# Kernel tuning notes

Measured on AMD Instinct MI355X. Metric: run time of the kernel, lower is better.

## Reference

```python
import jax, jax.numpy as jnp
import numpy as np
from jax import lax

B, H, W = 16, 512, 512
K, C, D = 64, 512, 256  # num_clusters, feature channels, descriptor_dim


def conv2d(x, w, b, stride, pad):
    y = lax.conv_general_dilated(x, w, (stride, stride), ((pad, pad), (pad, pad)),
                                 dimension_numbers=("NCHW", "OIHW", "NCHW"))
    return y + b[None, :, None, None]


def maxpool2(x):
    return lax.reduce_window(x, -jnp.inf, lax.max, (1, 1, 2, 2), (1, 1, 2, 2), "VALID")


def setup_inputs() -> dict:
    key = jax.random.key(0)
    ks = jax.random.split(key, 16)
    def rn(k, shape, fan_in):
        return jax.random.normal(k, shape, jnp.float32) * (1.0 / np.sqrt(fan_in))
    return {
        "x": jax.random.normal(ks[0], (B, 3, H, W), jnp.float32),
        "w1": rn(ks[1], (64, 3, 3, 3), 27), "b1": jnp.zeros((64,), jnp.float32),
        "w2": rn(ks[2], (128, 64, 3, 3), 576), "b2": jnp.zeros((128,), jnp.float32),
        "w3": rn(ks[3], (256, 128, 3, 3), 1152), "b3": jnp.zeros((256,), jnp.float32),
        "w4": rn(ks[4], (512, 256, 3, 3), 2304), "b4": jnp.zeros((512,), jnp.float32),
        "wv": rn(ks[5], (K, C), C), "bv": jnp.zeros((K,), jnp.float32),
        "centroids": jax.random.normal(ks[6], (K, C), jnp.float32),
        "fw1": rn(ks[7], (D, K * C), K * C), "fb1": jnp.zeros((D,), jnp.float32),
        "fw2": rn(ks[8], (D, D), D), "fb2": jnp.zeros((D,), jnp.float32),
    }


def reference(x, w1, b1, w2, b2, w3, b3, w4, b4, wv, bv, centroids, fw1, fb1, fw2, fb2):
    # conv backbone (SimpleGlobalDescriptor.backbone)
    h = jax.nn.relu(conv2d(x, w1, b1, 2, 1)); h = maxpool2(h)
    h = jax.nn.relu(conv2d(h, w2, b2, 2, 1)); h = maxpool2(h)
    h = jax.nn.relu(conv2d(h, w3, b3, 2, 1)); h = maxpool2(h)
    h = jax.nn.relu(conv2d(h, w4, b4, 2, 1))
    feats = jnp.mean(h, axis=(2, 3))  # AdaptiveAvgPool2d((1,1)) -> (B, C)
    # NetVLAD soft assignment: 1x1 conv + softmax over cluster dim
    logits = jnp.einsum("bc,kc->bk", feats, wv) + bv  # (B, K)
    a = jax.nn.softmax(logits, axis=1)  # spatial N == 1 after avgpool
    # fused VLAD: a[:,k] * (feats - centroids[k]) summed over N(=1)
    # == a (outer) feats - a[:,:,None] * centroids
    vlad = a[:, :, None] * (feats[:, None, :] - centroids[None, :, :])  # (B, K, C)
    v = vlad.reshape(B, K * C)
    # final descriptor MLP + L2 norm
    d = jax.nn.relu(v @ fw1.T + fb1) @ fw2.T + fb2
    d = d / jnp.linalg.norm(d, axis=1, keepdims=True)
    return d
```

## Files before the change

### kernel.cpp

```cpp
#include <hip/hip_runtime.h>
#include <hip/hip_bf16.h>

typedef unsigned short ushort_t;
typedef short bf16x8 __attribute__((ext_vector_type(8)));
typedef float f32x4 __attribute__((ext_vector_type(4)));

__device__ __forceinline__ ushort_t f2b(float f) {
    __hip_bfloat16 h = __float2bfloat16(f);
    return *reinterpret_cast<ushort_t*>(&h);
}
__device__ __forceinline__ float b2f(short v) {
    union { unsigned int u; float f; } cv;
    cv.u = ((unsigned int)(ushort_t)v) << 16;
    return cv.f;
}

__global__ __launch_bounds__(256) void k_packall(const float* __restrict__ w1,
                                                 const float* __restrict__ w2,
                                                 const float* __restrict__ w3,
                                                 const float* __restrict__ w4,
                                                 ushort_t* __restrict__ o1,
                                                 ushort_t* __restrict__ o2,
                                                 ushort_t* __restrict__ o3,
                                                 ushort_t* __restrict__ o4m) {
    const int bx = blockIdx.x;
    if (bx < 512) {
        const int co = bx;
        __shared__ float sw[2304];
        for (int i = threadIdx.x; i < 2304; i += 256) sw[i] = w4[(size_t)co * 2304 + i];
        __syncthreads();
        const int g = co >> 4, l15 = co & 15;
        for (int it = threadIdx.x; it < 288; it += 256) {
            const int kc = it >> 2, kg = it & 3;
            const int k0 = kc * 32 + kg * 8;
            const int tap = k0 >> 8, ci0 = k0 & 255;
            const int lane = kg * 16 + l15;
            ushort_t tmp[8];
#pragma unroll
            for (int j = 0; j < 8; ++j)
                tmp[j] = f2b(sw[(ci0 + j) * 9 + tap]);
            *(float4*)(o4m + ((size_t)(kc * 32 + g) * 64 + lane) * 8) = *(const float4*)tmp;
        }
    } else if (bx < 656) {
        const int slot = (bx - 512) * 256 + threadIdx.x;
        const int lane = slot & 63, g = (slot >> 6) & 15, kc = slot >> 10;
        const int k0 = kc * 32 + ((lane >> 4) << 3);
        const int tap = k0 >> 7, cib = k0 & 127;
        const int ky = tap >= 6 ? 2 : (tap >= 3 ? 1 : 0), kx = tap - ky * 3;
        const int co = g * 16 + (lane & 15);
#pragma unroll
        for (int j = 0; j < 8; ++j)
            o3[slot * 8 + j] = f2b(w3[((co * 128 + cib + j) * 3 + ky) * 3 + kx]);
    } else if (bx < 692) {
        const int slot = (bx - 656) * 256 + threadIdx.x;
        const int lane = slot & 63, g = (slot >> 6) & 7, kc = slot >> 9;
        const int k0 = kc * 32 + ((lane >> 4) << 3);
        const int tap = k0 >> 6, sb = k0 & 63;
        const int ky = tap >= 6 ? 2 : (tap >= 3 ? 1 : 0), kx = tap - ky * 3;
        const int co = g * 16 + (lane & 15);
#pragma unroll
        for (int j = 0; j < 8; ++j) {
            const int s = sb + j;
            const int ci = 16 * (s & 3) + (s >> 2);
            o2[slot * 8 + j] = f2b(w2[((co * 64 + ci) * 3 + ky) * 3 + kx]);
        }
    } else {
        const int slot = threadIdx.x;
        const int lane = slot & 63, nf = slot >> 6;
        const int co = nf * 16 + (lane & 15);
        const int kg = lane >> 4;
#pragma unroll
        for (int j = 0; j < 8; ++j) {
            const int k = kg * 8 + j;
            float v = 0.f;
            if (k < 24) {
                const int ky = k >> 3, q = k & 7;
                const int kx = q / 3, c = q - 3 * kx;
                v = w1[(co * 3 + c) * 9 + ky * 3 + kx];
            } else if (k < 27) {
                const int ky = k - 24;
                v = w1[(co * 3 + 2) * 9 + ky * 3 + 2];
            }
            o1[slot * 8 + j] = f2b(v);
        }
    }
}

__global__ __launch_bounds__(256) void k_conv1f(const float* __restrict__ x,
                                                const ushort_t* __restrict__ wpk1,
                                                const float* __restrict__ b1,
                                                ushort_t* __restrict__ y1) {
    const int rp = blockIdx.x, xh = blockIdx.y, b = blockIdx.z;
    const int tid = threadIdx.x;
    const int wid = tid >> 6, lane = tid & 63;
    const int l15 = lane & 15, kg = lane >> 4;

    __shared__ __align__(16) ushort_t sX[9 * 776];
    const float* xb = x + (size_t)b * 3 * 512 * 512;
    const int iy0 = 8 * rp - 1;
#pragma unroll
    for (int pass = 0; pass < 7; ++pass) {
        const int cr = pass * 4 + wid;
        if (cr < 27) {
            const int c = cr / 9, r = cr - 9 * (cr / 9);
            const int iy = iy0 + r;
            float4 q = {0.f, 0.f, 0.f, 0.f};
            if (iy >= 0)
                q = *(const float4*)(xb + ((size_t)c * 512 + iy) * 512 + 256 * xh + 4 * lane);
            const int base = r * 776 + (4 * lane + 1) * 3 + c;
            sX[base]     = f2b(q.x);
            sX[base + 3] = f2b(q.y);
            sX[base + 6] = f2b(q.z);
            sX[base + 9] = f2b(q.w);
        }
    }
    if (tid < 27) {
        const int c = tid / 9, r = tid - 9 * (tid / 9);
        const int iy = iy0 + r;
        const int ix = 256 * xh - 1;
        float v = (iy >= 0 && ix >= 0) ? xb[((size_t)c * 512 + iy) * 512 + ix] : 0.f;
        sX[r * 776 + c] = f2b(v);
    }
    __syncthreads();

    const int gq = l15 >> 2;
    const int dy = (l15 >> 1) & 1, dx = l15 & 1;

    bf16x8 bF[4];
    float bias[4];
#pragma unroll
    for (int nf = 0; nf < 4; ++nf) {
        bF[nf] = *reinterpret_cast<const bf16x8*>(wpk1 + (size_t)(nf * 64 + lane) * 8);
        bias[nf] = b1[nf * 16 + l15];
    }
    const f32x4 z4 = {0.f, 0.f, 0.f, 0.f};

#pragma unroll 4
    for (int it = 0; it < 8; ++it) {
        const int fl = wid * 8 + it;
        const int g2 = fl * 4 + gq;
        const int pyl = g2 >> 6, pxl = g2 & 63;
        const int cr = 2 * pyl + dy;
        const int oxl = 2 * pxl + dx;
        bf16x8 aF;
        if (kg < 3) {
            const int ba = (2 * cr + kg) * 776 + 6 * oxl;
            const unsigned int* pu = (const unsigned int*)(sX + ba);
            union { unsigned int u[4]; bf16x8 v; } cvt;
            cvt.u[0] = pu[0]; cvt.u[1] = pu[1]; cvt.u[2] = pu[2]; cvt.u[3] = pu[3];
            aF = cvt.v;
        } else {
            const int b0 = 2 * cr * 776 + 6 * oxl + 8;
            aF = (bf16x8){0, 0, 0, 0, 0, 0, 0, 0};
            aF[0] = (short)sX[b0];
            aF[1] = (short)sX[b0 + 776];
            aF[2] = (short)sX[b0 + 1552];
        }
        f32x4 acc[4];
#pragma unroll
        for (int nf = 0; nf < 4; ++nf)
            acc[nf] = __builtin_amdgcn_mfma_f32_16x16x32_bf16(aF, bF[nf], z4, 0, 0, 0);
        const int g_out = fl * 4 + kg;
        const int pyo = g_out >> 6, pxo = xh * 64 + (g_out & 63);
        union { ushort_t u[4]; uint2 v; } pk;
#pragma unroll
        for (int nf = 0; nf < 4; ++nf) {
            float v = fmaxf(fmaxf(acc[nf][0], acc[nf][1]), fmaxf(acc[nf][2], acc[nf][3]));
            pk.u[nf] = f2b(fmaxf(v + bias[nf], 0.f));
        }
        *(uint2*)(y1 + ((size_t)(b * 128 + 2 * rp + pyo) * 128 + pxo) * 64 + 4 * l15) = pk.v;
    }
}

__global__ __launch_bounds__(256) void k_conv2s(const ushort_t* __restrict__ y1,
                                                const ushort_t* __restrict__ wpk2,
                                                const float* __restrict__ b2,
                                                ushort_t* __restrict__ y2) {
    const int b = blockIdx.z;
    const int xq = blockIdx.y;
    const int rp = blockIdx.x;
    const int tid = threadIdx.x;
    const int wid = tid >> 6, lane = tid & 63;
    const int l15 = lane & 15, kg = lane >> 4;

    __shared__ __align__(16) ushort_t sY[170 * 72];
    bf16x8* sYv = (bf16x8*)sY;

    const ushort_t* xb = y1 + (size_t)b * 128 * 128 * 64;
    const int iyb = 4 * rp - 1, ixb = 32 * xq - 1;
    for (int j = tid; j < 1360; j += 256) {
        const int q = j & 7;
        const int pc = j >> 3;
        const int cc = pc % 34, r = pc / 34;
        const int iy = iyb + r, ix = ixb + cc;
        bf16x8 v = {0, 0, 0, 0, 0, 0, 0, 0};
        if (iy >= 0 && ix >= 0 && ix < 128)
            v = *reinterpret_cast<const bf16x8*>(xb + ((size_t)iy * 128 + ix) * 64 + q * 8);
        sYv[pc * 9 + (q ^ ((pc >> 1) & 7))] = v;
    }
    __syncthreads();

    const f32x4 z4 = {0.f, 0.f, 0.f, 0.f};
    f32x4 acc[2][2];
#pragma unroll
    for (int i = 0; i < 2; ++i) { acc[i][0] = z4; acc[i][1] = z4; }

#pragma unroll 1
    for (int tap = 0; tap < 9; ++tap) {
        const int ky = tap >= 6 ? 2 : (tap >= 3 ? 1 : 0), kx = tap - ky * 3;
#pragma unroll
        for (int h = 0; h < 2; ++h) {
            const int kc = tap * 2 + h;
            const int c8 = h * 4 + kg;
            bf16x8 aF[2];
#pragma unroll
            for (int oyi = 0; oyi < 2; ++oyi) {
                const int pc = (2 * oyi + ky) * 34 + 2 * l15 + kx;
                aF[oyi] = sYv[pc * 9 + (c8 ^ ((pc >> 1) & 7))];
            }
            bf16x8 bF[2];
#pragma unroll
            for (int nf = 0; nf < 2; ++nf)
                bF[nf] = *reinterpret_cast<const bf16x8*>(wpk2 + ((size_t)(kc * 8 + wid * 2 + nf) * 64 + lane) * 8);
#pragma unroll
            for (int oyi = 0; oyi < 2; ++oyi)
#pragma unroll
            for (int nf = 0; nf < 2; ++nf)
                acc[oyi][nf] = __builtin_amdgcn_mfma_f32_16x16x32_bf16(aF[oyi], bF[nf], acc[oyi][nf], 0, 0, 0);
        }
    }
#pragma unroll
    for (int nf = 0; nf < 2; ++nf) {
        const int co = wid * 32 + nf * 16 + l15;
        const float bias = b2[co];
#pragma unroll
        for (int p = 0; p < 2; ++p) {
            float v = fmaxf(fmaxf(acc[0][nf][2 * p], acc[0][nf][2 * p + 1]),
                            fmaxf(acc[1][nf][2 * p], acc[1][nf][2 * p + 1]));
            const int px = xq * 8 + kg * 2 + p;
            y2[((size_t)(b * 32 + rp) * 32 + px) * 128 + co] = f2b(fmaxf(v + bias, 0.f));
        }
    }
}

__global__ __launch_bounds__(256) void k_conv3m(const ushort_t* __restrict__ y2,
                                                const ushort_t* __restrict__ wpk3,
                                                const float* __restrict__ b3,
                                                ushort_t* __restrict__ y3) {
    const int gy = blockIdx.x, gn = blockIdx.y, b = blockIdx.z;
    const int oy0 = gy * 4;
    const int tid = threadIdx.x;
    const int wid = tid >> 6, lane = tid & 63;
    const int l15 = lane & 15, kl8 = (lane >> 4) << 3;
    const int g16 = gn * 4 + wid;
    const int co = g16 * 16 + l15;

    const ushort_t* xb = y2 + (size_t)b * 32 * 32 * 128;
    const f32x4 z4 = {0.f, 0.f, 0.f, 0.f};
    f32x4 acc[4] = {z4, z4, z4, z4};

#pragma unroll 1
    for (int tap = 0; tap < 9; ++tap) {
        const int ky = tap >= 6 ? 2 : (tap >= 3 ? 1 : 0), kx = tap - ky * 3;
        const int iyA = 2 * oy0 - 1 + ky;
        const int c = 2 * l15 - 1 + kx;
        const bool cok = (c >= 0);
#pragma unroll
        for (int h = 0; h < 4; ++h) {
            const int ci0 = h * 32;
            const int kc = tap * 4 + h;
            bf16x8 aF[4];
#pragma unroll
            for (int mf = 0; mf < 4; ++mf) {
                const int iy = iyA + 2 * mf;
                bf16x8 r = {0, 0, 0, 0, 0, 0, 0, 0};
                if (cok && iy >= 0) r = *reinterpret_cast<const bf16x8*>(xb + ((size_t)iy * 32 + c) * 128 + ci0 + kl8);
                aF[mf] = r;
            }
            const bf16x8 bF = *reinterpret_cast<const bf16x8*>(wpk3 + ((size_t)(kc * 16 + g16) * 64 + lane) * 8);
#pragma unroll
            for (int mf = 0; mf < 4; ++mf)
                acc[mf] = __builtin_amdgcn_mfma_f32_16x16x32_bf16(aF[mf], bF, acc[mf], 0, 0, 0);
        }
    }
    const int kg = lane >> 4;
    const float bias = b3[co];
#pragma unroll
    for (int mp = 0; mp < 2; ++mp) {
        const int py = gy * 2 + mp;
#pragma unroll
        for (int p = 0; p < 2; ++p) {
            float v = fmaxf(fmaxf(acc[2 * mp][2 * p], acc[2 * mp][2 * p + 1]),
                            fmaxf(acc[2 * mp + 1][2 * p], acc[2 * mp + 1][2 * p + 1]));
            const int px = kg * 2 + p;
            y3[((size_t)(b * 8 + py) * 8 + px) * 256 + co] = f2b(fmaxf(v + bias, 0.f));
        }
    }
}

__global__ __launch_bounds__(256) void k_conv4g(const ushort_t* __restrict__ y3,
                                                const ushort_t* __restrict__ wpk4m,
                                                const float* __restrict__ b4,
                                                float* __restrict__ feats) {
    const int g16 = blockIdx.x, b = blockIdx.y;
    const int tid = threadIdx.x, wid = tid >> 6, lane = tid & 63;
    const int l15 = lane & 15, kg = lane >> 4, kl8 = kg << 3;
    const int oy = l15 >> 2, ox = l15 & 3;
    const f32x4 z4 = {0.f, 0.f, 0.f, 0.f};
    f32x4 acc = z4;
    const ushort_t* yb = y3 + (size_t)b * 16384;
    const int kc0 = wid * 18;

#pragma unroll 3
    for (int i = 0; i < 18; ++i) {
        const int kc = kc0 + i;
        const int k0 = kc * 32 + kl8;
        const int tap = k0 >> 8, ci0 = k0 & 255;
        const int ky = tap / 3, kx = tap - 3 * (tap / 3);
        const int iy = 2 * oy - 1 + ky, ix = 2 * ox - 1 + kx;
        bf16x8 aF = {0, 0, 0, 0, 0, 0, 0, 0};
        if (iy >= 0 && ix >= 0)
            aF = *reinterpret_cast<const bf16x8*>(yb + ((iy * 8 + ix) << 8) + ci0);
        const bf16x8 bF = *reinterpret_cast<const bf16x8*>(wpk4m + ((size_t)(kc * 32 + g16) * 64 + lane) * 8);
        acc = __builtin_amdgcn_mfma_f32_16x16x32_bf16(aF, bF, acc, 0, 0, 0);
    }

    __shared__ f32x4 red[4][64];
    red[wid][lane] = acc;
    __syncthreads();
    if (wid == 0) {
        f32x4 t = red[0][lane];
        t = t + red[1][lane];
        t = t + red[2][lane];
        t = t + red[3][lane];
        const int co = g16 * 16 + l15;
        const float bias = b4[co];
        float s = fmaxf(t[0] + bias, 0.f) + fmaxf(t[1] + bias, 0.f)
                + fmaxf(t[2] + bias, 0.f) + fmaxf(t[3] + bias, 0.f);
        s += __shfl_xor(s, 16, 64);
        s += __shfl_xor(s, 32, 64);
        if (kg == 0) feats[b * 512 + co] = s * 0.0625f;
    }
}

__global__ __launch_bounds__(256) void k_head(const float* __restrict__ feats,
                                              const float* __restrict__ wv,
                                              const float* __restrict__ bv,
                                              const float* __restrict__ centroids,
                                              ushort_t* __restrict__ v) {
    const int b = blockIdx.x, sl8 = blockIdx.y;
    __shared__ float sf[512];
    __shared__ float sl[64];
    __shared__ float sa[64];
    for (int i = threadIdx.x; i < 512; i += 256) sf[i] = feats[b * 512 + i];
    __syncthreads();
    if (threadIdx.x < 64) {
        const int k = threadIdx.x;
        float s = bv[k];
        for (int c = 0; c < 512; ++c) s += sf[c] * wv[(size_t)k * 512 + c];
        sl[k] = s;
    }
    __syncthreads();
    if (threadIdx.x < 64) {
        const int k = threadIdx.x;
        float m = -1e30f;
        for (int i = 0; i < 64; ++i) m = fmaxf(m, sl[i]);
        float sum = 0.f;
        for (int i = 0; i < 64; ++i) sum += __expf(sl[i] - m);
        sa[k] = __expf(sl[k] - m) / sum;
    }
    __syncthreads();
    const int i4end = (sl8 + 1) * 4096;
    for (int i4 = sl8 * 4096 + threadIdx.x * 4; i4 < i4end; i4 += 1024) {
        const int k = i4 >> 9;
        const float a_ = sa[k];
        const float4 c4 = *(const float4*)(centroids + i4);
        const float4 f4 = *(const float4*)(&sf[i4 & 511]);
        union { ushort_t u[4]; uint2 w; } pk;
        pk.u[0] = f2b(a_ * (f4.x - c4.x));
        pk.u[1] = f2b(a_ * (f4.y - c4.y));
        pk.u[2] = f2b(a_ * (f4.z - c4.z));
        pk.u[3] = f2b(a_ * (f4.w - c4.w));
        *(uint2*)(v + (size_t)b * 32768 + i4) = pk.w;
    }
}

__global__ __launch_bounds__(256) void k_fc1m(const ushort_t* __restrict__ v,
                                              const float* __restrict__ fw1,
                                              float* __restrict__ part) {
    const int g16 = blockIdx.x, by = blockIdx.y;
    const int tid = threadIdx.x, wid = tid >> 6, lane = tid & 63;
    const int l15 = lane & 15, kg = lane >> 4;
    const f32x4 z4 = {0.f, 0.f, 0.f, 0.f};
    f32x4 acc = z4;
    const ushort_t* vrow = v + (size_t)l15 * 32768;
    const float* wrow = fw1 + (size_t)(g16 * 16 + l15) * 32768;
    const int kc0 = by * 16 + wid * 4;

#pragma unroll
    for (int i = 0; i < 4; ++i) {
        const int j0 = (kc0 + i) * 32 + kg * 8;
        const bf16x8 aF = *reinterpret_cast<const bf16x8*>(vrow + j0);
        const float4 wa = *(const float4*)(wrow + j0);
        const float4 wb = *(const float4*)(wrow + j0 + 4);
        bf16x8 bF;
        bF[0] = (short)f2b(wa.x); bF[1] = (short)f2b(wa.y);
        bF[2] = (short)f2b(wa.z); bF[3] = (short)f2b(wa.w);
        bF[4] = (short)f2b(wb.x); bF[5] = (short)f2b(wb.y);
        bF[6] = (short)f2b(wb.z); bF[7] = (short)f2b(wb.w);
        acc = __builtin_amdgcn_mfma_f32_16x16x32_bf16(aF, bF, acc, 0, 0, 0);
    }

    __shared__ f32x4 red[4][64];
    red[wid][lane] = acc;
    __syncthreads();
    if (wid == 0) {
        f32x4 t = red[0][lane];
        t = t + red[1][lane];
        t = t + red[2][lane];
        t = t + red[3][lane];
#pragma unroll
        for (int r = 0; r < 4; ++r)
            part[((size_t)by * 16 + (kg * 4 + r)) * 256 + g16 * 16 + l15] = t[r];
    }
}

__global__ __launch_bounds__(256) void k_fc2(const float* __restrict__ part,
                                             const float* __restrict__ fb1,
                                             const float* __restrict__ fw2,
                                             const float* __restrict__ fb2,
                                             float* __restrict__ out) {
    const int b = blockIdx.x;
    const int dd = threadIdx.x;
    __shared__ float sd[256];
    __shared__ float sq[256];
    float t = fb1[dd];
#pragma unroll 8
    for (int ks = 0; ks < 64; ++ks) t += part[((size_t)ks * 16 + b) * 256 + dd];
    sd[dd] = fmaxf(t, 0.f);
    __syncthreads();
    float s = fb2[dd];
    for (int j = 0; j < 256; ++j) s += sd[j] * fw2[(size_t)dd * 256 + j];
    sq[dd] = s * s;
    __syncthreads();
    for (int off = 128; off >= 1; off >>= 1) {
        if (dd < off) sq[dd] += sq[dd + off];
        __syncthreads();
    }
    const float inv = rsqrtf(sq[0]);
    out[b * 256 + dd] = s * inv;
}

extern "C" void kernel_launch(void* const* d_in, const int* in_sizes, int n_in,
                              void* d_out, int out_size, void* d_ws, size_t ws_size,
                              hipStream_t stream) {
    const float* x    = (const float*)d_in[0];
    const float* w1   = (const float*)d_in[1];
    const float* b1   = (const float*)d_in[2];
    const float* w2   = (const float*)d_in[3];
    const float* b2   = (const float*)d_in[4];
    const float* w3   = (const float*)d_in[5];
    const float* b3   = (const float*)d_in[6];
    const float* w4   = (const float*)d_in[7];
    const float* b4   = (const float*)d_in[8];
    const float* wv   = (const float*)d_in[9];
    const float* bv   = (const float*)d_in[10];
    const float* cen  = (const float*)d_in[11];
    const float* fw1  = (const float*)d_in[12];
    const float* fb1  = (const float*)d_in[13];
    const float* fw2  = (const float*)d_in[14];
    const float* fb2  = (const float*)d_in[15];
    float* out = (float*)d_out;

    char* p = (char*)d_ws;
    ushort_t* y1    = (ushort_t*)p; p += 33554432;
    ushort_t* wpk2  = (ushort_t*)p; p += 147456;
    ushort_t* wpk3  = (ushort_t*)p; p += 589824;
    ushort_t* wpk4m = (ushort_t*)p; p += 2359296;
    ushort_t* wpk1  = (ushort_t*)p; p += 4096;
    ushort_t* y2    = (ushort_t*)p; p += 4194304;
    ushort_t* y3    = (ushort_t*)p; p += 524288;
    float*    feats = (float*)p;    p += 32768;
    ushort_t* vbuf  = (ushort_t*)p; p += 1048576;
    float*    part  = (float*)p;    p += 1048576;

    k_packall<<<693, 256, 0, stream>>>(w1, w2, w3, w4, wpk1, wpk2, wpk3, wpk4m);
    k_conv1f<<<dim3(64, 2, 16), 256, 0, stream>>>(x, wpk1, b1, y1);
    k_conv2s<<<dim3(32, 4, 16), 256, 0, stream>>>(y1, wpk2, b2, y2);
    k_conv3m<<<dim3(4, 4, 16), 256, 0, stream>>>(y2, wpk3, b3, y3);
    k_conv4g<<<dim3(32, 16), 256, 0, stream>>>(y3, wpk4m, b4, feats);
    k_head<<<dim3(16, 8), 256, 0, stream>>>(feats, wv, bv, cen, vbuf);
    k_fc1m<<<dim3(16, 64), 256, 0, stream>>>(vbuf, fw1, part);
    k_fc2<<<16, 256, 0, stream>>>(part, fb1, fw2, fb2, out);
}
```

Baseline: 109.7 us.

## Split conv3 rows across more blocks and parallelize head and fc2 reductions

conv3 now computes two output rows per block instead of four and launches twice as many blocks, which raises occupancy on a small grid. The NetVLAD logit dot products in the head now use all 256 threads, each taking a quarter of the channels, followed by a shared-memory reduction. fc2 moves to 1024-thread blocks that split both the partial-sum accumulation and the 256x256 matvec four ways. In exchange, weight fragments are reloaded more often in conv3, and the extra shared-memory reductions add synchronisation.

```diff
diff --git a/kernel.cpp b/kernel.cpp
--- a/kernel.cpp
+++ b/kernel.cpp
@@ -248,7 +248,7 @@
                                                 const float* __restrict__ b3,
                                                 ushort_t* __restrict__ y3) {
     const int gy = blockIdx.x, gn = blockIdx.y, b = blockIdx.z;
-    const int oy0 = gy * 4;
+    const int oy0 = gy * 2;
     const int tid = threadIdx.x;
     const int wid = tid >> 6, lane = tid & 63;
     const int l15 = lane & 15, kl8 = (lane >> 4) << 3;
@@ -257,7 +257,7 @@
 
     const ushort_t* xb = y2 + (size_t)b * 32 * 32 * 128;
     const f32x4 z4 = {0.f, 0.f, 0.f, 0.f};
-    f32x4 acc[4] = {z4, z4, z4, z4};
+    f32x4 acc[2] = {z4, z4};
 
 #pragma unroll 1
     for (int tap = 0; tap < 9; ++tap) {
@@ -269,9 +269,9 @@
         for (int h = 0; h < 4; ++h) {
             const int ci0 = h * 32;
             const int kc = tap * 4 + h;
-            bf16x8 aF[4];
-#pragma unroll
-            for (int mf = 0; mf < 4; ++mf) {
+            bf16x8 aF[2];
+#pragma unroll
+            for (int mf = 0; mf < 2; ++mf) {
                 const int iy = iyA + 2 * mf;
                 bf16x8 r = {0, 0, 0, 0, 0, 0, 0, 0};
                 if (cok && iy >= 0) r = *reinterpret_cast<const bf16x8*>(xb + ((size_t)iy * 32 + c) * 128 + ci0 + kl8);
@@ -279,22 +279,18 @@
             }
             const bf16x8 bF = *reinterpret_cast<const bf16x8*>(wpk3 + ((size_t)(kc * 16 + g16) * 64 + lane) * 8);
 #pragma unroll
-            for (int mf = 0; mf < 4; ++mf)
+            for (int mf = 0; mf < 2; ++mf)
                 acc[mf] = __builtin_amdgcn_mfma_f32_16x16x32_bf16(aF[mf], bF, acc[mf], 0, 0, 0);
         }
     }
     const int kg = lane >> 4;
     const float bias = b3[co];
 #pragma unroll
-    for (int mp = 0; mp < 2; ++mp) {
-        const int py = gy * 2 + mp;
-#pragma unroll
-        for (int p = 0; p < 2; ++p) {
-            float v = fmaxf(fmaxf(acc[2 * mp][2 * p], acc[2 * mp][2 * p + 1]),
-                            fmaxf(acc[2 * mp + 1][2 * p], acc[2 * mp + 1][2 * p + 1]));
-            const int px = kg * 2 + p;
-            y3[((size_t)(b * 8 + py) * 8 + px) * 256 + co] = f2b(fmaxf(v + bias, 0.f));
-        }
+    for (int p = 0; p < 2; ++p) {
+        float v = fmaxf(fmaxf(acc[0][2 * p], acc[0][2 * p + 1]),
+                        fmaxf(acc[1][2 * p], acc[1][2 * p + 1]));
+        const int px = kg * 2 + p;
+        y3[((size_t)(b * 8 + gy) * 8 + px) * 256 + co] = f2b(fmaxf(v + bias, 0.f));
     }
 }
 
@@ -350,15 +346,22 @@
                                               ushort_t* __restrict__ v) {
     const int b = blockIdx.x, sl8 = blockIdx.y;
     __shared__ float sf[512];
+    __shared__ float plog[4][64];
     __shared__ float sl[64];
     __shared__ float sa[64];
     for (int i = threadIdx.x; i < 512; i += 256) sf[i] = feats[b * 512 + i];
     __syncthreads();
+    {
+        const int k = threadIdx.x & 63, q = threadIdx.x >> 6;
+        float s = 0.f;
+        const int c0 = q * 128;
+        for (int c = c0; c < c0 + 128; ++c) s += sf[c] * wv[(size_t)k * 512 + c];
+        plog[q][k] = s;
+    }
+    __syncthreads();
     if (threadIdx.x < 64) {
         const int k = threadIdx.x;
-        float s = bv[k];
-        for (int c = 0; c < 512; ++c) s += sf[c] * wv[(size_t)k * 512 + c];
-        sl[k] = s;
+        sl[k] = plog[0][k] + plog[1][k] + plog[2][k] + plog[3][k] + bv[k];
     }
     __syncthreads();
     if (threadIdx.x < 64) {
@@ -425,30 +428,41 @@
     }
 }
 
-__global__ __launch_bounds__(256) void k_fc2(const float* __restrict__ part,
-                                             const float* __restrict__ fb1,
-                                             const float* __restrict__ fw2,
-                                             const float* __restrict__ fb2,
-                                             float* __restrict__ out) {
+__global__ __launch_bounds__(1024) void k_fc2(const float* __restrict__ part,
+                                              const float* __restrict__ fb1,
+                                              const float* __restrict__ fw2,
+                                              const float* __restrict__ fb2,
+                                              float* __restrict__ out) {
     const int b = blockIdx.x;
-    const int dd = threadIdx.x;
+    const int tid = threadIdx.x;
+    const int dd = tid & 255, jq = tid >> 8;
     __shared__ float sd[256];
+    __shared__ float pr[4][256];
     __shared__ float sq[256];
-    float t = fb1[dd];
-#pragma unroll 8
-    for (int ks = 0; ks < 64; ++ks) t += part[((size_t)ks * 16 + b) * 256 + dd];
-    sd[dd] = fmaxf(t, 0.f);
-    __syncthreads();
-    float s = fb2[dd];
-    for (int j = 0; j < 256; ++j) s += sd[j] * fw2[(size_t)dd * 256 + j];
-    sq[dd] = s * s;
+    float t = 0.f;
+    const int ks0 = jq * 16;
+    for (int ks = ks0; ks < ks0 + 16; ++ks) t += part[((size_t)ks * 16 + b) * 256 + dd];
+    pr[jq][dd] = t;
+    __syncthreads();
+    if (jq == 0)
+        sd[dd] = fmaxf(pr[0][dd] + pr[1][dd] + pr[2][dd] + pr[3][dd] + fb1[dd], 0.f);
+    __syncthreads();
+    float s = 0.f;
+    const int j0 = jq * 64;
+    for (int j = j0; j < j0 + 64; ++j) s += sd[j] * fw2[(size_t)dd * 256 + j];
+    pr[jq][dd] = s;
+    __syncthreads();
+    float sfull = 0.f;
+    if (jq == 0) {
+        sfull = pr[0][dd] + pr[1][dd] + pr[2][dd] + pr[3][dd] + fb2[dd];
+        sq[dd] = sfull * sfull;
+    }
     __syncthreads();
     for (int off = 128; off >= 1; off >>= 1) {
-        if (dd < off) sq[dd] += sq[dd + off];
+        if (jq == 0 && dd < off) sq[dd] += sq[dd + off];
         __syncthreads();
     }
-    const float inv = rsqrtf(sq[0]);
-    out[b * 256 + dd] = s * inv;
+    if (jq == 0) out[b * 256 + dd] = sfull * rsqrtf(sq[0]);
 }
 
 extern "C" void kernel_launch(void* const* d_in, const int* in_sizes, int n_in,
@@ -487,9 +501,9 @@
     k_packall<<<693, 256, 0, stream>>>(w1, w2, w3, w4, wpk1, wpk2, wpk3, wpk4m);
     k_conv1f<<<dim3(64, 2, 16), 256, 0, stream>>>(x, wpk1, b1, y1);
     k_conv2s<<<dim3(32, 4, 16), 256, 0, stream>>>(y1, wpk2, b2, y2);
-    k_conv3m<<<dim3(4, 4, 16), 256, 0, stream>>>(y2, wpk3, b3, y3);
+    k_conv3m<<<dim3(8, 4, 16), 256, 0, stream>>>(y2, wpk3, b3, y3);
     k_conv4g<<<dim3(32, 16), 256, 0, stream>>>(y3, wpk4m, b4, feats);
     k_head<<<dim3(16, 8), 256, 0, stream>>>(feats, wv, bv, cen, vbuf);
     k_fc1m<<<dim3(16, 64), 256, 0, stream>>>(vbuf, fw1, part);
-    k_fc2<<<16, 256, 0, stream>>>(part, fb1, fw2, fb2, out);
-}
+    k_fc2<<<16, 1024, 0, stream>>>(part, fb1, fw2, fb2, out);
+}
```

After: 104.1 us, median of 2. 5.1% less time.
